# Kernel tuning notes

Hardware: AMD Instinct MI355X
Metric: run time of the kernel (lower is better)

The kernel has to match this reference:

```python
import jax, jax.numpy as jnp
import numpy as np
import math

SEGMENT_LENGTHS = [2048, 4096, 8192]
DILATION_RATES = [1, 2, 4]


def setup_inputs() -> dict:
    key = jax.random.key(0)
    kq, kk, kv = jax.random.split(key, 3)
    b, n, h, d = 2, 8192, 32, 128
    q = jax.random.normal(kq, (b, n, h, d), dtype=jnp.float32)
    k = jax.random.normal(kk, (b, n, h, d), dtype=jnp.float32)
    v = jax.random.normal(kv, (b, n, h, d), dtype=jnp.float32)
    return {"q": q, "k": k, "v": v}


def _dilated_attention(q, k, v):
    # Faithful translation of _compute_dilated_attention.
    # NOTE: torch.matmul on (b, S, h, d) with transpose(-2, -1) contracts over
    # head_dim d and yields (b, S, h, h) scores: heads attend to heads at a
    # single (possibly dilated) key position. We reproduce that exactly.
    b, n, h, d = q.shape
    scale = 1.0 / math.sqrt(d)
    out = jnp.zeros_like(q)
    for seg_len, dil in zip(SEGMENT_LENGTHS, DILATION_RATES):
        if seg_len > n:
            continue
        n_seg = n // seg_len
        cov = n_seg * seg_len
        # (b, n_seg, seg_len, h, d)
        qs = q[:, :cov].reshape(b, n_seg, seg_len, h, d)
        if dil == 1:
            ks = k[:, :cov].reshape(b, n_seg, seg_len, h, d)
            vs = v[:, :cov].reshape(b, n_seg, seg_len, h, d)
        else:
            # idx[g, i] = g*seg_len + i*dil, clamped to n-1 (matches the loop)
            idx = (jnp.arange(n_seg)[:, None] * seg_len
                   + jnp.arange(seg_len)[None, :] * dil)
            idx = jnp.minimum(idx, n - 1)  # (n_seg, seg_len)
            ks = k[:, idx]  # (b, n_seg, seg_len, h, d)
            vs = v[:, idx]
        scores = jnp.einsum('bgsid,bgsjd->bgsij', qs, ks) * scale  # (b,g,s,h,h)
        attn = jax.nn.softmax(scores, axis=-1)
        res = jnp.einsum('bgsij,bgsjd->bgsid', attn, vs)
        # later configs overwrite earlier ones, as in the torch loop
        out = out.at[:, :cov].set(res.reshape(b, cov, h, d))
    return out


def reference(q, k, v):
    # world_size == 1 -> hierarchy level 1 -> _local_forward with all heads
    # local, which is just _compute_dilated_attention.
    return _dilated_attention(q, k, v)
```

## Files before the change

kernel.cpp:

```cpp
#include <hip/hip_runtime.h>
#include <hip/hip_bf16.h>

typedef __attribute__((ext_vector_type(4))) float f32x4;
typedef __attribute__((ext_vector_type(8))) __bf16 bf16x8;

#define NCTX 8192
#define DH 128
#define ROWE 4096
#define SC2 0.12751705766482797f
#define KSTR 136
#define PSTR 40
#define OSTR 132
#define BUFS (32*KSTR)

__device__ __forceinline__ unsigned f2bf(float x) {
  union { float f; unsigned u; } un; un.f = x;
  return (un.u + 0x7FFFu + ((un.u >> 16) & 1u)) >> 16;
}
__device__ __forceinline__ unsigned pk2(float a, float b) {
  float2 t; t.x = a; t.y = b;
  union { __hip_bfloat162 h; unsigned u; } un;
  un.h = __float22bfloat162_rn(t);
  return un.u;
}

template<bool NT>
__device__ __forceinline__ void stage_row(const float* __restrict__ src,
                                          unsigned short* dst, int lane) {
  const int jb = lane >> 5, d = 4 * (lane & 31);
#pragma unroll
  for (int half = 0; half < 2; ++half) {
    f32x4 x[8];
#pragma unroll
    for (int ch = 0; ch < 8; ++ch) {
      const f32x4* p = reinterpret_cast<const f32x4*>(src + 4*lane + 256*(half*8 + ch));
      x[ch] = NT ? __builtin_nontemporal_load(p) : *p;
    }
#pragma unroll
    for (int ch = 0; ch < 8; ++ch) {
      const int j = jb + 2*(half*8 + ch);
      uint2 wv;
      wv.x = pk2(x[ch][0], x[ch][1]);
      wv.y = pk2(x[ch][2], x[ch][3]);
      *reinterpret_cast<uint2*>(&dst[j*KSTR + d]) = wv;
    }
  }
}

__global__ __launch_bounds__(256, 4) void hda(
    const float* __restrict__ q, const float* __restrict__ kg,
    const float* __restrict__ v, float* __restrict__ out)
{
  extern __shared__ __align__(16) unsigned short lds[];

  const int tid  = threadIdx.x;
  const int w    = tid >> 6;
  const int lane = tid & 63;
  const int c = lane & 15;
  const int g = lane >> 4;
  const int jb = lane >> 5, dcol = 4 * (lane & 31);

  const int pos = blockIdx.x * 4 + w;
  const int b = pos >> 13;
  const int s = pos & (NCTX - 1);
  const int r = min(4 * s, NCTX - 1);

  const float* qb_ = q  + (size_t)b * NCTX * ROWE;
  const float* kb_ = kg + (size_t)b * NCTX * ROWE;
  const float* vb_ = v  + (size_t)b * NCTX * ROWE;
  float*       op  = out + ((size_t)b * NCTX + s) * ROWE;

  unsigned short* sb = lds + w * BUFS;

  stage_row<true>(qb_ + (size_t)s * ROWE, sb, lane);
  bf16x8 qa[2][4];
#pragma unroll
  for (int t = 0; t < 2; ++t)
#pragma unroll
    for (int ks = 0; ks < 4; ++ks)
      qa[t][ks] = *reinterpret_cast<const bf16x8*>(&sb[(t*16 + c)*KSTR + ks*32 + g*8]);

  stage_row<false>(kb_ + (size_t)r * ROWE, sb, lane);
  bf16x8 kf[2][4];
#pragma unroll
  for (int t = 0; t < 2; ++t)
#pragma unroll
    for (int ks = 0; ks < 4; ++ks)
      kf[t][ks] = *reinterpret_cast<const bf16x8*>(&sb[(t*16 + c)*KSTR + ks*32 + g*8]);

  const float* vsrc = vb_ + (size_t)r * ROWE;
  f32x4 vx[8];
#pragma unroll
  for (int ch = 0; ch < 8; ++ch)
    vx[ch] = *reinterpret_cast<const f32x4*>(vsrc + 4*lane + 256*ch);
  __builtin_amdgcn_sched_barrier(0);

  f32x4 S[2][2];
#pragma unroll
  for (int it = 0; it < 2; ++it)
#pragma unroll
    for (int jt = 0; jt < 2; ++jt) {
      f32x4 acc = (f32x4)0.0f;
#pragma unroll
      for (int ks = 0; ks < 4; ++ks)
        acc = __builtin_amdgcn_mfma_f32_16x16x32_bf16(qa[it][ks], kf[jt][ks], acc, 0, 0, 0);
      S[it][jt] = acc;
    }

#pragma unroll
  for (int ch = 0; ch < 8; ++ch) {
    uint2 wv;
    wv.x = pk2(vx[ch][0], vx[ch][1]);
    wv.y = pk2(vx[ch][2], vx[ch][3]);
    *reinterpret_cast<uint2*>(&sb[(jb + 2*ch)*KSTR + dcol]) = wv;
  }
#pragma unroll
  for (int ch = 0; ch < 8; ++ch)
    vx[ch] = *reinterpret_cast<const f32x4*>(vsrc + 4*lane + 256*(8 + ch));
  __builtin_amdgcn_sched_barrier(0);

  float p[2][2][4], inv[2][4];
#pragma unroll
  for (int it = 0; it < 2; ++it) {
    float ls[4] = {0.f, 0.f, 0.f, 0.f};
#pragma unroll
    for (int jt = 0; jt < 2; ++jt)
#pragma unroll
      for (int rr = 0; rr < 4; ++rr) {
        float e = exp2f(S[it][jt][rr] * SC2);
        p[it][jt][rr] = e;
        ls[rr] += e;
      }
#pragma unroll
    for (int m = 1; m <= 8; m <<= 1)
#pragma unroll
      for (int rr = 0; rr < 4; ++rr)
        ls[rr] += __shfl_xor(ls[rr], m);
#pragma unroll
    for (int rr = 0; rr < 4; ++rr) inv[it][rr] = 1.0f / ls[rr];
  }

#pragma unroll
  for (int ch = 0; ch < 8; ++ch) {
    uint2 wv;
    wv.x = pk2(vx[ch][0], vx[ch][1]);
    wv.y = pk2(vx[ch][2], vx[ch][3]);
    *reinterpret_cast<uint2*>(&sb[(jb + 2*(8 + ch))*KSTR + dcol]) = wv;
  }

  bf16x8 va[8];
#pragma unroll
  for (int dt = 0; dt < 8; ++dt) {
    unsigned t0 = sb[(g*8 + 0)*KSTR + dt*16 + c];
    unsigned t1 = sb[(g*8 + 1)*KSTR + dt*16 + c];
    unsigned t2 = sb[(g*8 + 2)*KSTR + dt*16 + c];
    unsigned t3 = sb[(g*8 + 3)*KSTR + dt*16 + c];
    unsigned t4 = sb[(g*8 + 4)*KSTR + dt*16 + c];
    unsigned t5 = sb[(g*8 + 5)*KSTR + dt*16 + c];
    unsigned t6 = sb[(g*8 + 6)*KSTR + dt*16 + c];
    unsigned t7 = sb[(g*8 + 7)*KSTR + dt*16 + c];
    union { unsigned u[4]; bf16x8 f; } un;
    un.u[0] = t0 | (t1 << 16); un.u[1] = t2 | (t3 << 16);
    un.u[2] = t4 | (t5 << 16); un.u[3] = t6 | (t7 << 16);
    va[dt] = un.f;
  }

#pragma unroll
  for (int it = 0; it < 2; ++it)
#pragma unroll
    for (int jt = 0; jt < 2; ++jt)
#pragma unroll
      for (int rr = 0; rr < 4; ++rr)
        sb[(it*16 + g*4 + rr)*PSTR + jt*16 + c] =
            (unsigned short)f2bf(p[it][jt][rr] * inv[it][rr]);

  bf16x8 pa[2];
  pa[0] = *reinterpret_cast<const bf16x8*>(&sb[c*PSTR + g*8]);
  pa[1] = *reinterpret_cast<const bf16x8*>(&sb[(16 + c)*PSTR + g*8]);

  float* ob = reinterpret_cast<float*>(sb);
#pragma unroll
  for (int it = 0; it < 2; ++it) {
    f32x4 o[8];
#pragma unroll
    for (int dt = 0; dt < 8; ++dt)
      o[dt] = __builtin_amdgcn_mfma_f32_16x16x32_bf16(va[dt], pa[it], (f32x4)0.0f, 0, 0, 0);
#pragma unroll
    for (int dt = 0; dt < 8; ++dt)
      *reinterpret_cast<f32x4*>(&ob[c*OSTR + dt*16 + g*4]) = o[dt];
#pragma unroll
    for (int ch = 0; ch < 8; ++ch) {
      const int flat = 4*lane + 256*ch;
      const int row = flat >> 7, col = flat & 127;
      f32x4 y = *reinterpret_cast<const f32x4*>(&ob[row*OSTR + col]);
      __builtin_nontemporal_store(y, reinterpret_cast<f32x4*>(op + it*2048 + flat));
    }
  }
}

extern "C" void kernel_launch(void* const* d_in, const int* in_sizes, int n_in,
                              void* d_out, int out_size, void* d_ws, size_t ws_size,
                              hipStream_t stream) {
  const float* q = (const float*)d_in[0];
  const float* k = (const float*)d_in[1];
  const float* v = (const float*)d_in[2];
  float* o = (float*)d_out;
  hda<<<dim3(4096, 1, 1), dim3(256, 1, 1), 4 * BUFS * 2, stream>>>(q, k, v, o);
}
```

Baseline: 123.0 us.

## Split positions into private-key and shared-clamped-key paths, reuse K/V across rows

Positions s < 2048 still load their own K/V row at 4*s. Positions s >= 2048 all use the clamped last row, so those warps stage K/V once and loop over 8 query half-rows (16 heads each), prefetching the next Q chunk into registers. This cuts redundant K/V reads for three quarters of the positions and reduces the block count. Occupancy is lowered to 3 blocks per CU.

```diff
diff --git a/kernel.cpp b/kernel.cpp
--- a/kernel.cpp
+++ b/kernel.cpp
@@ -12,6 +12,9 @@
 #define PSTR 40
 #define OSTR 132
 #define BUFS (32*KSTR)
+#define NPRIV 1024
+#define NSHRD 768
+#define ITERS 8
 
 __device__ __forceinline__ unsigned f2bf(float x) {
   union { float f; unsigned u; } un; un.f = x;
@@ -47,7 +50,26 @@
   }
 }
 
-__global__ __launch_bounds__(256, 4) void hda(
+__device__ __forceinline__ void gather_va(const unsigned short* vbuf,
+                                          bf16x8* va, int c, int g) {
+#pragma unroll
+  for (int dt = 0; dt < 8; ++dt) {
+    unsigned t0 = vbuf[(g*8 + 0)*KSTR + dt*16 + c];
+    unsigned t1 = vbuf[(g*8 + 1)*KSTR + dt*16 + c];
+    unsigned t2 = vbuf[(g*8 + 2)*KSTR + dt*16 + c];
+    unsigned t3 = vbuf[(g*8 + 3)*KSTR + dt*16 + c];
+    unsigned t4 = vbuf[(g*8 + 4)*KSTR + dt*16 + c];
+    unsigned t5 = vbuf[(g*8 + 5)*KSTR + dt*16 + c];
+    unsigned t6 = vbuf[(g*8 + 6)*KSTR + dt*16 + c];
+    unsigned t7 = vbuf[(g*8 + 7)*KSTR + dt*16 + c];
+    union { unsigned u[4]; bf16x8 f; } un;
+    un.u[0] = t0 | (t1 << 16); un.u[1] = t2 | (t3 << 16);
+    un.u[2] = t4 | (t5 << 16); un.u[3] = t6 | (t7 << 16);
+    va[dt] = un.f;
+  }
+}
+
+__global__ __launch_bounds__(256, 3) void hda(
     const float* __restrict__ q, const float* __restrict__ kg,
     const float* __restrict__ v, float* __restrict__ out)
 {
@@ -60,27 +82,140 @@
   const int g = lane >> 4;
   const int jb = lane >> 5, dcol = 4 * (lane & 31);
 
-  const int pos = blockIdx.x * 4 + w;
-  const int b = pos >> 13;
-  const int s = pos & (NCTX - 1);
-  const int r = min(4 * s, NCTX - 1);
-
-  const float* qb_ = q  + (size_t)b * NCTX * ROWE;
-  const float* kb_ = kg + (size_t)b * NCTX * ROWE;
-  const float* vb_ = v  + (size_t)b * NCTX * ROWE;
-  float*       op  = out + ((size_t)b * NCTX + s) * ROWE;
-
   unsigned short* sb = lds + w * BUFS;
 
-  stage_row<true>(qb_ + (size_t)s * ROWE, sb, lane);
-  bf16x8 qa[2][4];
-#pragma unroll
-  for (int t = 0; t < 2; ++t)
-#pragma unroll
-    for (int ks = 0; ks < 4; ++ks)
-      qa[t][ks] = *reinterpret_cast<const bf16x8*>(&sb[(t*16 + c)*KSTR + ks*32 + g*8]);
-
-  stage_row<false>(kb_ + (size_t)r * ROWE, sb, lane);
+  if (blockIdx.x < NPRIV) {
+    const int p = blockIdx.x * 4 + w;
+    const int b = p >> 11;
+    const int s = p & 2047;
+    const int r = 4 * s;
+
+    const float* qsrc = q  + ((size_t)b * NCTX + s) * ROWE;
+    const float* ksrc = kg + ((size_t)b * NCTX + r) * ROWE;
+    const float* vsrc = v  + ((size_t)b * NCTX + r) * ROWE;
+    float*       op   = out + ((size_t)b * NCTX + s) * ROWE;
+
+    stage_row<true>(qsrc, sb, lane);
+    bf16x8 qa[2][4];
+#pragma unroll
+    for (int t = 0; t < 2; ++t)
+#pragma unroll
+      for (int ks = 0; ks < 4; ++ks)
+        qa[t][ks] = *reinterpret_cast<const bf16x8*>(&sb[(t*16 + c)*KSTR + ks*32 + g*8]);
+
+    stage_row<false>(ksrc, sb, lane);
+    bf16x8 kf[2][4];
+#pragma unroll
+    for (int t = 0; t < 2; ++t)
+#pragma unroll
+      for (int ks = 0; ks < 4; ++ks)
+        kf[t][ks] = *reinterpret_cast<const bf16x8*>(&sb[(t*16 + c)*KSTR + ks*32 + g*8]);
+
+    f32x4 vx[8];
+#pragma unroll
+    for (int ch = 0; ch < 8; ++ch)
+      vx[ch] = *reinterpret_cast<const f32x4*>(vsrc + 4*lane + 256*ch);
+    __builtin_amdgcn_sched_barrier(0);
+
+    f32x4 S[2][2];
+#pragma unroll
+    for (int it = 0; it < 2; ++it)
+#pragma unroll
+      for (int jt = 0; jt < 2; ++jt) {
+        f32x4 acc = (f32x4)0.0f;
+#pragma unroll
+        for (int ks = 0; ks < 4; ++ks)
+          acc = __builtin_amdgcn_mfma_f32_16x16x32_bf16(qa[it][ks], kf[jt][ks], acc, 0, 0, 0);
+        S[it][jt] = acc;
+      }
+
+#pragma unroll
+    for (int ch = 0; ch < 8; ++ch) {
+      uint2 wv;
+      wv.x = pk2(vx[ch][0], vx[ch][1]);
+      wv.y = pk2(vx[ch][2], vx[ch][3]);
+      *reinterpret_cast<uint2*>(&sb[(jb + 2*ch)*KSTR + dcol]) = wv;
+    }
+#pragma unroll
+    for (int ch = 0; ch < 8; ++ch)
+      vx[ch] = *reinterpret_cast<const f32x4*>(vsrc + 4*lane + 256*(8 + ch));
+    __builtin_amdgcn_sched_barrier(0);
+
+    float pp[2][2][4], inv[2][4];
+#pragma unroll
+    for (int it = 0; it < 2; ++it) {
+      float ls[4] = {0.f, 0.f, 0.f, 0.f};
+#pragma unroll
+      for (int jt = 0; jt < 2; ++jt)
+#pragma unroll
+        for (int rr = 0; rr < 4; ++rr) {
+          float e = exp2f(S[it][jt][rr] * SC2);
+          pp[it][jt][rr] = e;
+          ls[rr] += e;
+        }
+#pragma unroll
+      for (int m = 1; m <= 8; m <<= 1)
+#pragma unroll
+        for (int rr = 0; rr < 4; ++rr)
+          ls[rr] += __shfl_xor(ls[rr], m);
+#pragma unroll
+      for (int rr = 0; rr < 4; ++rr) inv[it][rr] = 1.0f / ls[rr];
+    }
+
+#pragma unroll
+    for (int ch = 0; ch < 8; ++ch) {
+      uint2 wv;
+      wv.x = pk2(vx[ch][0], vx[ch][1]);
+      wv.y = pk2(vx[ch][2], vx[ch][3]);
+      *reinterpret_cast<uint2*>(&sb[(jb + 2*(8 + ch))*KSTR + dcol]) = wv;
+    }
+
+    bf16x8 va[8];
+    gather_va(sb, va, c, g);
+
+#pragma unroll
+    for (int it = 0; it < 2; ++it)
+#pragma unroll
+      for (int jt = 0; jt < 2; ++jt)
+#pragma unroll
+        for (int rr = 0; rr < 4; ++rr)
+          sb[(it*16 + g*4 + rr)*PSTR + jt*16 + c] =
+              (unsigned short)f2bf(pp[it][jt][rr] * inv[it][rr]);
+
+    bf16x8 pa[2];
+    pa[0] = *reinterpret_cast<const bf16x8*>(&sb[c*PSTR + g*8]);
+    pa[1] = *reinterpret_cast<const bf16x8*>(&sb[(16 + c)*PSTR + g*8]);
+
+    float* ob = reinterpret_cast<float*>(sb);
+#pragma unroll
+    for (int it = 0; it < 2; ++it) {
+      f32x4 o[8];
+#pragma unroll
+      for (int dt = 0; dt < 8; ++dt)
+        o[dt] = __builtin_amdgcn_mfma_f32_16x16x32_bf16(va[dt], pa[it], (f32x4)0.0f, 0, 0, 0);
+#pragma unroll
+      for (int dt = 0; dt < 8; ++dt)
+        *reinterpret_cast<f32x4*>(&ob[c*OSTR + dt*16 + g*4]) = o[dt];
+#pragma unroll
+      for (int ch = 0; ch < 8; ++ch) {
+        const int flat = 4*lane + 256*ch;
+        const int row = flat >> 7, col = flat & 127;
+        f32x4 y = *reinterpret_cast<const f32x4*>(&ob[row*OSTR + col]);
+        __builtin_nontemporal_store(y, reinterpret_cast<f32x4*>(op + it*2048 + flat));
+      }
+    }
+    return;
+  }
+
+  const int gw = (blockIdx.x - NPRIV) * 4 + w;
+  const int b  = (gw >= 1536) ? 1 : 0;
+  const size_t frbase = (size_t)(gw - b*1536) * 128;
+  const float* qbase = q   + ((size_t)b*262144 + 65536 + frbase) * DH;
+  float*       obase = out + ((size_t)b*262144 + 65536 + frbase) * DH;
+  const float* k8 = kg + ((size_t)b * NCTX + (NCTX-1)) * ROWE;
+  const float* v8 = v  + ((size_t)b * NCTX + (NCTX-1)) * ROWE;
+
+  stage_row<false>(k8, sb, lane);
   bf16x8 kf[2][4];
 #pragma unroll
   for (int t = 0; t < 2; ++t)
@@ -88,47 +223,58 @@
     for (int ks = 0; ks < 4; ++ks)
       kf[t][ks] = *reinterpret_cast<const bf16x8*>(&sb[(t*16 + c)*KSTR + ks*32 + g*8]);
 
-  const float* vsrc = vb_ + (size_t)r * ROWE;
-  f32x4 vx[8];
-#pragma unroll
-  for (int ch = 0; ch < 8; ++ch)
-    vx[ch] = *reinterpret_cast<const f32x4*>(vsrc + 4*lane + 256*ch);
-  __builtin_amdgcn_sched_barrier(0);
-
-  f32x4 S[2][2];
-#pragma unroll
-  for (int it = 0; it < 2; ++it)
+  stage_row<false>(v8, sb, lane);
+  bf16x8 va[8];
+  gather_va(sb, va, c, g);
+
+  {
+    f32x4 x[8];
+#pragma unroll
+    for (int ch = 0; ch < 8; ++ch)
+      x[ch] = __builtin_nontemporal_load(
+          reinterpret_cast<const f32x4*>(qbase + 4*lane + 256*ch));
+#pragma unroll
+    for (int ch = 0; ch < 8; ++ch) {
+      uint2 wv;
+      wv.x = pk2(x[ch][0], x[ch][1]);
+      wv.y = pk2(x[ch][2], x[ch][3]);
+      *reinterpret_cast<uint2*>(&sb[(jb + 2*ch)*KSTR + dcol]) = wv;
+    }
+  }
+
+  f32x4 pf[8];
+#pragma unroll 1
+  for (int iter = 0; iter < ITERS; ++iter) {
+    bf16x8 qa[4];
+#pragma unroll
+    for (int ks = 0; ks < 4; ++ks)
+      qa[ks] = *reinterpret_cast<const bf16x8*>(&sb[c*KSTR + ks*32 + g*8]);
+
+    if (iter + 1 < ITERS) {
+#pragma unroll
+      for (int ch = 0; ch < 8; ++ch)
+        pf[ch] = __builtin_nontemporal_load(reinterpret_cast<const f32x4*>(
+            qbase + (size_t)(iter + 1) * 2048 + 4*lane + 256*ch));
+      __builtin_amdgcn_sched_barrier(0);
+    }
+
+    f32x4 S[2];
 #pragma unroll
     for (int jt = 0; jt < 2; ++jt) {
       f32x4 acc = (f32x4)0.0f;
 #pragma unroll
       for (int ks = 0; ks < 4; ++ks)
-        acc = __builtin_amdgcn_mfma_f32_16x16x32_bf16(qa[it][ks], kf[jt][ks], acc, 0, 0, 0);
-      S[it][jt] = acc;
-    }
-
-#pragma unroll
-  for (int ch = 0; ch < 8; ++ch) {
-    uint2 wv;
-    wv.x = pk2(vx[ch][0], vx[ch][1]);
-    wv.y = pk2(vx[ch][2], vx[ch][3]);
-    *reinterpret_cast<uint2*>(&sb[(jb + 2*ch)*KSTR + dcol]) = wv;
-  }
-#pragma unroll
-  for (int ch = 0; ch < 8; ++ch)
-    vx[ch] = *reinterpret_cast<const f32x4*>(vsrc + 4*lane + 256*(8 + ch));
-  __builtin_amdgcn_sched_barrier(0);
-
-  float p[2][2][4], inv[2][4];
-#pragma unroll
-  for (int it = 0; it < 2; ++it) {
-    float ls[4] = {0.f, 0.f, 0.f, 0.f};
+        acc = __builtin_amdgcn_mfma_f32_16x16x32_bf16(qa[ks], kf[jt][ks], acc, 0, 0, 0);
+      S[jt] = acc;
+    }
+
+    float pp[2][4], ls[4] = {0.f, 0.f, 0.f, 0.f};
 #pragma unroll
     for (int jt = 0; jt < 2; ++jt)
 #pragma unroll
       for (int rr = 0; rr < 4; ++rr) {
-        float e = exp2f(S[it][jt][rr] * SC2);
-        p[it][jt][rr] = e;
+        float e = exp2f(S[jt][rr] * SC2);
+        pp[jt][rr] = e;
         ls[rr] += e;
       }
 #pragma unroll
@@ -136,55 +282,23 @@
 #pragma unroll
       for (int rr = 0; rr < 4; ++rr)
         ls[rr] += __shfl_xor(ls[rr], m);
-#pragma unroll
-    for (int rr = 0; rr < 4; ++rr) inv[it][rr] = 1.0f / ls[rr];
-  }
-
-#pragma unroll
-  for (int ch = 0; ch < 8; ++ch) {
-    uint2 wv;
-    wv.x = pk2(vx[ch][0], vx[ch][1]);
-    wv.y = pk2(vx[ch][2], vx[ch][3]);
-    *reinterpret_cast<uint2*>(&sb[(jb + 2*(8 + ch))*KSTR + dcol]) = wv;
-  }
-
-  bf16x8 va[8];
-#pragma unroll
-  for (int dt = 0; dt < 8; ++dt) {
-    unsigned t0 = sb[(g*8 + 0)*KSTR + dt*16 + c];
-    unsigned t1 = sb[(g*8 + 1)*KSTR + dt*16 + c];
-    unsigned t2 = sb[(g*8 + 2)*KSTR + dt*16 + c];
-    unsigned t3 = sb[(g*8 + 3)*KSTR + dt*16 + c];
-    unsigned t4 = sb[(g*8 + 4)*KSTR + dt*16 + c];
-    unsigned t5 = sb[(g*8 + 5)*KSTR + dt*16 + c];
-    unsigned t6 = sb[(g*8 + 6)*KSTR + dt*16 + c];
-    unsigned t7 = sb[(g*8 + 7)*KSTR + dt*16 + c];
-    union { unsigned u[4]; bf16x8 f; } un;
-    un.u[0] = t0 | (t1 << 16); un.u[1] = t2 | (t3 << 16);
-    un.u[2] = t4 | (t5 << 16); un.u[3] = t6 | (t7 << 16);
-    va[dt] = un.f;
-  }
-
-#pragma unroll
-  for (int it = 0; it < 2; ++it)
+    float inv[4];
+#pragma unroll
+    for (int rr = 0; rr < 4; ++rr) inv[rr] = 1.0f / ls[rr];
+
 #pragma unroll
     for (int jt = 0; jt < 2; ++jt)
 #pragma unroll
       for (int rr = 0; rr < 4; ++rr)
-        sb[(it*16 + g*4 + rr)*PSTR + jt*16 + c] =
-            (unsigned short)f2bf(p[it][jt][rr] * inv[it][rr]);
-
-  bf16x8 pa[2];
-  pa[0] = *reinterpret_cast<const bf16x8*>(&sb[c*PSTR + g*8]);
-  pa[1] = *reinterpret_cast<const bf16x8*>(&sb[(16 + c)*PSTR + g*8]);
-
-  float* ob = reinterpret_cast<float*>(sb);
-#pragma unroll
-  for (int it = 0; it < 2; ++it) {
+        sb[(g*4 + rr)*PSTR + jt*16 + c] =
+            (unsigned short)f2bf(pp[jt][rr] * inv[rr]);
+    bf16x8 pa = *reinterpret_cast<const bf16x8*>(&sb[c*PSTR + g*8]);
+
     f32x4 o[8];
 #pragma unroll
     for (int dt = 0; dt < 8; ++dt)
-      o[dt] = __builtin_amdgcn_mfma_f32_16x16x32_bf16(va[dt], pa[it], (f32x4)0.0f, 0, 0, 0);
+      o[dt] = __builtin_amdgcn_mfma_f32_16x16x32_bf16(va[dt], pa, (f32x4)0.0f, 0, 0, 0);
+    float* ob = reinterpret_cast<float*>(sb);
 #pragma unroll
     for (int dt = 0; dt < 8; ++dt)
       *reinterpret_cast<f32x4*>(&ob[c*OSTR + dt*16 + g*4]) = o[dt];
@@ -193,7 +307,18 @@
       const int flat = 4*lane + 256*ch;
       const int row = flat >> 7, col = flat & 127;
       f32x4 y = *reinterpret_cast<const f32x4*>(&ob[row*OSTR + col]);
-      __builtin_nontemporal_store(y, reinterpret_cast<f32x4*>(op + it*2048 + flat));
+      __builtin_nontemporal_store(y, reinterpret_cast<f32x4*>(
+          obase + (size_t)iter * 2048 + flat));
+    }
+
+    if (iter + 1 < ITERS) {
+#pragma unroll
+      for (int ch = 0; ch < 8; ++ch) {
+        uint2 wv;
+        wv.x = pk2(pf[ch][0], pf[ch][1]);
+        wv.y = pk2(pf[ch][2], pf[ch][3]);
+        *reinterpret_cast<uint2*>(&sb[(jb + 2*ch)*KSTR + dcol]) = wv;
+      }
     }
   }
 }
@@ -205,5 +330,5 @@
   const float* k = (const float*)d_in[1];
   const float* v = (const float*)d_in[2];
   float* o = (float*)d_out;
-  hda<<<dim3(4096, 1, 1), dim3(256, 1, 1), 4 * BUFS * 2, stream>>>(q, k, v, o);
-}
+  hda<<<dim3(NPRIV + NSHRD, 1, 1), dim3(256, 1, 1), 4 * BUFS * 2, stream>>>(q, k, v, o);
+}
```

Result: faster. 118.1 us (-4.0%).

## Share clamped last K/V row across block and store output directly from MFMA

Applied to the files above, without the earlier changes.

For positions with s>=2048 the clamped key index is always the last row, so each block stages that K row and a transposed V row once into shared LDS and skips per-wave K/V global loads and conversions. The output epilogue drops the LDS transpose and writes MFMA results straight to global with nontemporal stores. LDS usage grows and launch bounds drop to 3 waves per SIMD, which lowers occupancy; the direct stores are less coalesced.

```diff
diff --git a/kernel.cpp b/kernel.cpp
--- a/kernel.cpp
+++ b/kernel.cpp
@@ -10,7 +10,7 @@
 #define SC2 0.12751705766482797f
 #define KSTR 136
 #define PSTR 40
-#define OSTR 132
+#define VTSTR 40
 #define BUFS (32*KSTR)
 
 __device__ __forceinline__ unsigned f2bf(float x) {
@@ -47,7 +47,7 @@
   }
 }
 
-__global__ __launch_bounds__(256, 4) void hda(
+__global__ __launch_bounds__(256, 3) void hda(
     const float* __restrict__ q, const float* __restrict__ kg,
     const float* __restrict__ v, float* __restrict__ out)
 {
@@ -64,6 +64,8 @@
   const int b = pos >> 13;
   const int s = pos & (NCTX - 1);
   const int r = min(4 * s, NCTX - 1);
+  const int s0 = (blockIdx.x * 4) & (NCTX - 1);
+  const bool shared_kv = (s0 >= 2048);
 
   const float* qb_ = q  + (size_t)b * NCTX * ROWE;
   const float* kb_ = kg + (size_t)b * NCTX * ROWE;
@@ -71,6 +73,29 @@
   float*       op  = out + ((size_t)b * NCTX + s) * ROWE;
 
   unsigned short* sb = lds + w * BUFS;
+  const unsigned short* kbuf = shared_kv ? (lds + 4*BUFS) : sb;
+  unsigned short* vt = lds + 5*BUFS;
+
+  if (shared_kv) {
+    const float* kr8 = kb_ + (size_t)(NCTX - 1) * ROWE;
+    const float* vr8 = vb_ + (size_t)(NCTX - 1) * ROWE;
+    const int d0 = 4 * (tid & 31), jj = tid >> 5;
+#pragma unroll
+    for (int ch = 0; ch < 4; ++ch) {
+      const int fo = 4*tid + 1024*ch;
+      const int j  = jj + 8*ch;
+      f32x4 xk = *reinterpret_cast<const f32x4*>(kr8 + fo);
+      f32x4 xv = *reinterpret_cast<const f32x4*>(vr8 + fo);
+      uint2 wk;
+      wk.x = pk2(xk[0], xk[1]); wk.y = pk2(xk[2], xk[3]);
+      *reinterpret_cast<uint2*>(&lds[4*BUFS + j*KSTR + d0]) = wk;
+      vt[(d0 + 0)*VTSTR + j] = (unsigned short)f2bf(xv[0]);
+      vt[(d0 + 1)*VTSTR + j] = (unsigned short)f2bf(xv[1]);
+      vt[(d0 + 2)*VTSTR + j] = (unsigned short)f2bf(xv[2]);
+      vt[(d0 + 3)*VTSTR + j] = (unsigned short)f2bf(xv[3]);
+    }
+    __syncthreads();
+  }
 
   stage_row<true>(qb_ + (size_t)s * ROWE, sb, lane);
   bf16x8 qa[2][4];
@@ -80,20 +105,23 @@
     for (int ks = 0; ks < 4; ++ks)
       qa[t][ks] = *reinterpret_cast<const bf16x8*>(&sb[(t*16 + c)*KSTR + ks*32 + g*8]);
 
-  stage_row<false>(kb_ + (size_t)r * ROWE, sb, lane);
+  if (!shared_kv)
+    stage_row<false>(kb_ + (size_t)r * ROWE, sb, lane);
   bf16x8 kf[2][4];
 #pragma unroll
   for (int t = 0; t < 2; ++t)
 #pragma unroll
     for (int ks = 0; ks < 4; ++ks)
-      kf[t][ks] = *reinterpret_cast<const bf16x8*>(&sb[(t*16 + c)*KSTR + ks*32 + g*8]);
+      kf[t][ks] = *reinterpret_cast<const bf16x8*>(&kbuf[(t*16 + c)*KSTR + ks*32 + g*8]);
 
   const float* vsrc = vb_ + (size_t)r * ROWE;
   f32x4 vx[8];
-#pragma unroll
-  for (int ch = 0; ch < 8; ++ch)
-    vx[ch] = *reinterpret_cast<const f32x4*>(vsrc + 4*lane + 256*ch);
-  __builtin_amdgcn_sched_barrier(0);
+  if (!shared_kv) {
+#pragma unroll
+    for (int ch = 0; ch < 8; ++ch)
+      vx[ch] = *reinterpret_cast<const f32x4*>(vsrc + 4*lane + 256*ch);
+    __builtin_amdgcn_sched_barrier(0);
+  }
 
   f32x4 S[2][2];
 #pragma unroll
@@ -107,17 +135,19 @@
       S[it][jt] = acc;
     }
 
-#pragma unroll
-  for (int ch = 0; ch < 8; ++ch) {
-    uint2 wv;
-    wv.x = pk2(vx[ch][0], vx[ch][1]);
-    wv.y = pk2(vx[ch][2], vx[ch][3]);
-    *reinterpret_cast<uint2*>(&sb[(jb + 2*ch)*KSTR + dcol]) = wv;
-  }
-#pragma unroll
-  for (int ch = 0; ch < 8; ++ch)
-    vx[ch] = *reinterpret_cast<const f32x4*>(vsrc + 4*lane + 256*(8 + ch));
-  __builtin_amdgcn_sched_barrier(0);
+  if (!shared_kv) {
+#pragma unroll
+    for (int ch = 0; ch < 8; ++ch) {
+      uint2 wv;
+      wv.x = pk2(vx[ch][0], vx[ch][1]);
+      wv.y = pk2(vx[ch][2], vx[ch][3]);
+      *reinterpret_cast<uint2*>(&sb[(jb + 2*ch)*KSTR + dcol]) = wv;
+    }
+#pragma unroll
+    for (int ch = 0; ch < 8; ++ch)
+      vx[ch] = *reinterpret_cast<const f32x4*>(vsrc + 4*lane + 256*(8 + ch));
+    __builtin_amdgcn_sched_barrier(0);
+  }
 
   float p[2][2][4], inv[2][4];
 #pragma unroll
@@ -140,29 +170,37 @@
     for (int rr = 0; rr < 4; ++rr) inv[it][rr] = 1.0f / ls[rr];
   }
 
-#pragma unroll
-  for (int ch = 0; ch < 8; ++ch) {
-    uint2 wv;
-    wv.x = pk2(vx[ch][0], vx[ch][1]);
-    wv.y = pk2(vx[ch][2], vx[ch][3]);
-    *reinterpret_cast<uint2*>(&sb[(jb + 2*(8 + ch))*KSTR + dcol]) = wv;
+  if (!shared_kv) {
+#pragma unroll
+    for (int ch = 0; ch < 8; ++ch) {
+      uint2 wv;
+      wv.x = pk2(vx[ch][0], vx[ch][1]);
+      wv.y = pk2(vx[ch][2], vx[ch][3]);
+      *reinterpret_cast<uint2*>(&sb[(jb + 2*(8 + ch))*KSTR + dcol]) = wv;
+    }
   }
 
   bf16x8 va[8];
-#pragma unroll
-  for (int dt = 0; dt < 8; ++dt) {
-    unsigned t0 = sb[(g*8 + 0)*KSTR + dt*16 + c];
-    unsigned t1 = sb[(g*8 + 1)*KSTR + dt*16 + c];
-    unsigned t2 = sb[(g*8 + 2)*KSTR + dt*16 + c];
-    unsigned t3 = sb[(g*8 + 3)*KSTR + dt*16 + c];
-    unsigned t4 = sb[(g*8 + 4)*KSTR + dt*16 + c];
-    unsigned t5 = sb[(g*8 + 5)*KSTR + dt*16 + c];
-    unsigned t6 = sb[(g*8 + 6)*KSTR + dt*16 + c];
-    unsigned t7 = sb[(g*8 + 7)*KSTR + dt*16 + c];
-    union { unsigned u[4]; bf16x8 f; } un;
-    un.u[0] = t0 | (t1 << 16); un.u[1] = t2 | (t3 << 16);
-    un.u[2] = t4 | (t5 << 16); un.u[3] = t6 | (t7 << 16);
-    va[dt] = un.f;
+  if (shared_kv) {
+#pragma unroll
+    for (int dt = 0; dt < 8; ++dt)
+      va[dt] = *reinterpret_cast<const bf16x8*>(&vt[(dt*16 + c)*VTSTR + g*8]);
+  } else {
+#pragma unroll
+    for (int dt = 0; dt < 8; ++dt) {
+      unsigned t0 = sb[(g*8 + 0)*KSTR + dt*16 + c];
+      unsigned t1 = sb[(g*8 + 1)*KSTR + dt*16 + c];
+      unsigned t2 = sb[(g*8 + 2)*KSTR + dt*16 + c];
+      unsigned t3 = sb[(g*8 + 3)*KSTR + dt*16 + c];
+      unsigned t4 = sb[(g*8 + 4)*KSTR + dt*16 + c];
+      unsigned t5 = sb[(g*8 + 5)*KSTR + dt*16 + c];
+      unsigned t6 = sb[(g*8 + 6)*KSTR + dt*16 + c];
+      unsigned t7 = sb[(g*8 + 7)*KSTR + dt*16 + c];
+      union { unsigned u[4]; bf16x8 f; } un;
+      un.u[0] = t0 | (t1 << 16); un.u[1] = t2 | (t3 << 16);
+      un.u[2] = t4 | (t5 << 16); un.u[3] = t6 | (t7 << 16);
+      va[dt] = un.f;
+    }
   }
 
 #pragma unroll
@@ -178,7 +216,6 @@
   pa[0] = *reinterpret_cast<const bf16x8*>(&sb[c*PSTR + g*8]);
   pa[1] = *reinterpret_cast<const bf16x8*>(&sb[(16 + c)*PSTR + g*8]);
 
-  float* ob = reinterpret_cast<float*>(sb);
 #pragma unroll
   for (int it = 0; it < 2; ++it) {
     f32x4 o[8];
@@ -187,14 +224,8 @@
       o[dt] = __builtin_amdgcn_mfma_f32_16x16x32_bf16(va[dt], pa[it], (f32x4)0.0f, 0, 0, 0);
 #pragma unroll
     for (int dt = 0; dt < 8; ++dt)
-      *reinterpret_cast<f32x4*>(&ob[c*OSTR + dt*16 + g*4]) = o[dt];
-#pragma unroll
-    for (int ch = 0; ch < 8; ++ch) {
-      const int flat = 4*lane + 256*ch;
-      const int row = flat >> 7, col = flat & 127;
-      f32x4 y = *reinterpret_cast<const f32x4*>(&ob[row*OSTR + col]);
-      __builtin_nontemporal_store(y, reinterpret_cast<f32x4*>(op + it*2048 + flat));
-    }
+      __builtin_nontemporal_store(o[dt],
+          reinterpret_cast<f32x4*>(op + (it*16 + c)*DH + dt*16 + g*4));
   }
 }
 
@@ -205,5 +236,6 @@
   const float* k = (const float*)d_in[1];
   const float* v = (const float*)d_in[2];
   float* o = (float*)d_out;
-  hda<<<dim3(4096, 1, 1), dim3(256, 1, 1), 4 * BUFS * 2, stream>>>(q, k, v, o);
-}
+  const size_t ldsz = (size_t)(5 * BUFS + 128 * VTSTR) * 2;
+  hda<<<dim3(4096, 1, 1), dim3(256, 1, 1), ldsz, stream>>>(q, k, v, o);
+}
```

New measurement: 134.7 us. +9.5%, slower.
